# Performance work log

Hardware: AMD Instinct MI355X
Metric: run time of the kernel (lower is better)

## Reference

```python
import jax, jax.numpy as jnp
import numpy as np

N_NODES = 50000
N_EDGES = 800000
IN_DIM = 128
HIDDEN = 128
NUM_CLASSES = 2
NUM_GRAPHS = 512


def _linear_params(key, fan_in, fan_out):
    # torch nn.Linear default init: U(-1/sqrt(fan_in), 1/sqrt(fan_in))
    k1, k2 = jax.random.split(key)
    bound = 1.0 / np.sqrt(fan_in)
    W = jax.random.uniform(k1, (fan_in, fan_out), jnp.float32, -bound, bound)
    b = jax.random.uniform(k2, (fan_out,), jnp.float32, -bound, bound)
    return W, b


def setup_inputs() -> dict:
    key = jax.random.key(0)
    ks = jax.random.split(key, 8)
    x = jax.random.normal(ks[0], (N_NODES, IN_DIM), jnp.float32)
    edge_index = jax.random.randint(ks[1], (2, N_EDGES), 0, N_NODES, jnp.int64)
    batch = jnp.sort(jax.random.randint(ks[2], (N_NODES,), 0, NUM_GRAPHS, jnp.int64))
    W1a, b1a = _linear_params(ks[3], IN_DIM, HIDDEN)
    W1b, b1b = _linear_params(ks[4], HIDDEN, HIDDEN)
    W2a, b2a = _linear_params(ks[5], HIDDEN, HIDDEN)
    W2b, b2b = _linear_params(ks[6], HIDDEN, HIDDEN)
    Wfc, bfc = _linear_params(ks[7], HIDDEN, NUM_CLASSES)
    return {"x": x, "edge_index": edge_index, "batch": batch,
            "W1a": W1a, "b1a": b1a, "W1b": W1b, "b1b": b1b,
            "W2a": W2a, "b2a": b2a, "W2b": W2b, "b2b": b2b,
            "Wfc": Wfc, "bfc": bfc}


def _gin_layer(x, src, dst, Wa, ba, Wb, bb):
    # GINConv (eps=0): h_i = MLP(x_i + sum_{j->i} x_j)
    agg = jax.ops.segment_sum(x[src], dst, num_segments=N_NODES)
    h = x + agg
    h = jax.nn.relu(h @ Wa + ba)
    h = h @ Wb + bb
    return jax.nn.relu(h)  # outer F.relu in forward; dropout is identity (eval)


def reference(x, edge_index, batch, W1a, b1a, W1b, b1b, W2a, b2a, W2b, b2b, Wfc, bfc):
    src, dst = edge_index[0], edge_index[1]
    h = _gin_layer(x, src, dst, W1a, b1a, W1b, b1b)
    h = _gin_layer(h, src, dst, W2a, b2a, W2b, b2b)
    # global mean pool per graph
    sums = jax.ops.segment_sum(h, batch, num_segments=NUM_GRAPHS)
    counts = jax.ops.segment_sum(jnp.ones((N_NODES,), h.dtype), batch, num_segments=NUM_GRAPHS)
    g_emb = sums / jnp.maximum(counts, 1.0)[:, None]
    return g_emb @ Wfc + bfc  # [NUM_GRAPHS, NUM_CLASSES]
```

## Files before the change

kernel.cpp:

```cpp
#include <hip/hip_runtime.h>

typedef unsigned short ushort_t;
typedef unsigned int uint_t;

typedef __bf16 bf16x8 __attribute__((ext_vector_type(8)));
typedef float f32x4 __attribute__((ext_vector_type(4)));

#define N_NODES 50000
#define N_EDGES 800000
#define DIM 128
#define NUM_GRAPHS 512
#define LDA 136

#define ELL_CAP 64

#define EDGE_GROUPS 8
#define EDGE_BUCKET ((N_NODES + EDGE_GROUPS - 1) / EDGE_GROUPS)
#define EDGE_CHUNK 2048
#define EDGE_CHUNKS ((N_EDGES + EDGE_CHUNK - 1) / EDGE_CHUNK)
#define EDGE_BLOCKS (EDGE_CHUNKS * EDGE_GROUPS)

#define PREP_X_BLOCKS 6250
#define PREP_W_BLOCKS 256
#define PREP_B_BLOCKS 196
#define PREP_TOTAL (EDGE_BLOCKS + PREP_X_BLOCKS + PREP_W_BLOCKS + PREP_B_BLOCKS + 1)

__device__ __forceinline__ float bf2f(ushort_t u) {
    return __uint_as_float(((uint_t)u) << 16);
}
__device__ __forceinline__ ushort_t f2bf(float f) {
    uint_t u = __float_as_uint(f);
    u = (u + 0x7FFF + ((u >> 16) & 1)) >> 16;
    return (ushort_t)u;
}
__device__ __forceinline__ bf16x8 as_bf16x8(uint4 v) {
    return __builtin_bit_cast(bf16x8, v);
}

__global__ void zero_detect_kernel(int* cnt, float* gsum, const void* xraw,
                                   const void* eiraw, int* flags) {
    int i = blockIdx.x * 256 + threadIdx.x;
    if (i < N_NODES) cnt[i] = 0;
    if (i < NUM_GRAPHS * DIM) gsum[i] = 0.f;
    if (i == 0) {
        const ushort_t* u = (const ushort_t*)xraw;
        int extreme = 0;
        for (int k = 0; k < 128; ++k) {
            int e = (u[k] >> 7) & 0xFF;
            if (e >= 0xC0) extreme++;
        }
        flags[0] = (extreme > 8) ? 1 : 0;
        const int* p = (const int*)eiraw;
        int nonzero = 0;
        for (int k = 1; k < 64; k += 2) nonzero += (p[k] != 0);
        flags[1] = (nonzero == 0) ? 1 : 0;
    }
}

__global__ __launch_bounds__(256) void prep_all_kernel(
    const void* xraw, const void* braw, const void* eiraw,
    const void* W0, const void* W1, const void* W2, const void* W3,
    const void* pb1a, const void* pb1b, const void* pb2a, const void* pb2b,
    const void* pWfc, const void* pbfc, const int* __restrict__ flags,
    ushort_t* __restrict__ xout, ushort_t* __restrict__ wpout,
    int* __restrict__ batch32, float* __restrict__ params,
    int* __restrict__ cnt, int* __restrict__ ell) {
    int b = blockIdx.x;
    int tid = threadIdx.x;
    if (b < EDGE_BLOCKS) {
        int group = b & (EDGE_GROUPS - 1);
        int chunk = b >> 3;
        int lo = group * EDGE_BUCKET;
        int hi = lo + EDGE_BUCKET;
        const int* p = (const int*)eiraw;
        int i64 = flags[1];
#pragma unroll
        for (int i = 0; i < EDGE_CHUNK; i += 256) {
            int e = chunk * EDGE_CHUNK + i + tid;
            if (e < N_EDGES) {
                int d = i64 ? p[2 * (N_EDGES + e)] : p[N_EDGES + e];
                if (d >= lo && d < hi) {
                    int s = i64 ? p[2 * e] : p[e];
                    int slot = atomicAdd(&cnt[d], 1);
                    if (slot < ELL_CAP) ell[d * ELL_CAP + slot] = s;
                }
            }
        }
    } else if (b < EDGE_BLOCKS + PREP_X_BLOCKS) {
        if (flags[0]) {
            int i = (b - EDGE_BLOCKS) * 256 + tid;
            if (i < N_NODES * DIM / 4) {
                float4 v = ((const float4*)xraw)[i];
                ushort4 o;
                o.x = f2bf(v.x); o.y = f2bf(v.y); o.z = f2bf(v.z); o.w = f2bf(v.w);
                ((ushort4*)xout)[i] = o;
            }
        }
    } else if (b < EDGE_BLOCKS + PREP_X_BLOCKS + PREP_W_BLOCKS) {
        int gidx = (b - EDGE_BLOCKS - PREP_X_BLOCKS) * 256 + tid;
        int which = gidx >> 14;
        const void* W = (which == 0) ? W0 : (which == 1) ? W1 : (which == 2) ? W2 : W3;
        int idx = gidx & 16383;
        int j = idx & 7;
        int L = (idx >> 3) & 63;
        int t = (idx >> 9) & 7;
        int s = idx >> 12;
        int k = s * 32 + (L >> 4) * 8 + j;
        int n = t * 16 + (L & 15);
        int off = k * DIM + n;
        wpout[gidx] = flags[0] ? f2bf(((const float*)W)[off]) : ((const ushort_t*)W)[off];
    } else if (b < EDGE_BLOCKS + PREP_X_BLOCKS + PREP_W_BLOCKS + PREP_B_BLOCKS) {
        int i = (b - EDGE_BLOCKS - PREP_X_BLOCKS - PREP_W_BLOCKS) * 256 + tid;
        if (i < N_NODES) {
            const int* p = (const int*)braw;
            batch32[i] = flags[1] ? p[2 * i] : p[i];
        }
    } else {
        for (int i = tid; i < 770; i += 256) {
            const void* srcp;
            int j;
            if (i < 128)      { srcp = pb1a; j = i; }
            else if (i < 256) { srcp = pb1b; j = i - 128; }
            else if (i < 384) { srcp = pb2a; j = i - 256; }
            else if (i < 512) { srcp = pb2b; j = i - 384; }
            else if (i < 768) { srcp = pWfc; j = i - 512; }
            else              { srcp = pbfc; j = i - 768; }
            params[i] = flags[0] ? ((const float*)srcp)[j] : bf2f(((const ushort_t*)srcp)[j]);
        }
    }
}

__global__ __launch_bounds__(256) void agg_kernel(const ushort_t* __restrict__ featA,
                                                  const void* __restrict__ featB,
                                                  const int* __restrict__ flags,
                                                  const int* __restrict__ deg,
                                                  const int* __restrict__ ell,
                                                  ushort_t* __restrict__ hout) {
    int n = blockIdx.x * 16 + (threadIdx.x >> 4);
    int lane = threadIdx.x & 15;
    if (n >= N_NODES) return;
    const ushort_t* feat = featA;
    if (flags && !flags[0]) feat = (const ushort_t*)featB;
    const uint4* fp = reinterpret_cast<const uint4*>(feat);
    uint4 v = fp[(size_t)n * 16 + lane];
    float a0 = bf2f((ushort_t)(v.x & 0xffff));
    float a1 = bf2f((ushort_t)(v.x >> 16));
    float a2 = bf2f((ushort_t)(v.y & 0xffff));
    float a3 = bf2f((ushort_t)(v.y >> 16));
    float a4 = bf2f((ushort_t)(v.z & 0xffff));
    float a5 = bf2f((ushort_t)(v.z >> 16));
    float a6 = bf2f((ushort_t)(v.w & 0xffff));
    float a7 = bf2f((ushort_t)(v.w >> 16));
    int e1 = deg[n];
    if (e1 > ELL_CAP) e1 = ELL_CAP;
    const int* __restrict__ row = ell + (size_t)n * ELL_CAP;
    int j = 0;
#define ACC8(V) \
    a0 += bf2f((ushort_t)((V).x & 0xffff)); a1 += bf2f((ushort_t)((V).x >> 16)); \
    a2 += bf2f((ushort_t)((V).y & 0xffff)); a3 += bf2f((ushort_t)((V).y >> 16)); \
    a4 += bf2f((ushort_t)((V).z & 0xffff)); a5 += bf2f((ushort_t)((V).z >> 16)); \
    a6 += bf2f((ushort_t)((V).w & 0xffff)); a7 += bf2f((ushort_t)((V).w >> 16));
    for (; j + 8 <= e1; j += 8) {
        int s0 = row[j],     s1 = row[j + 1], s2 = row[j + 2], s3 = row[j + 3];
        int s4 = row[j + 4], s5 = row[j + 5], s6 = row[j + 6], s7 = row[j + 7];
        uint4 g0 = fp[(size_t)s0 * 16 + lane];
        uint4 g1 = fp[(size_t)s1 * 16 + lane];
        uint4 g2 = fp[(size_t)s2 * 16 + lane];
        uint4 g3 = fp[(size_t)s3 * 16 + lane];
        uint4 g4 = fp[(size_t)s4 * 16 + lane];
        uint4 g5 = fp[(size_t)s5 * 16 + lane];
        uint4 g6 = fp[(size_t)s6 * 16 + lane];
        uint4 g7 = fp[(size_t)s7 * 16 + lane];
        ACC8(g0) ACC8(g1) ACC8(g2) ACC8(g3)
        ACC8(g4) ACC8(g5) ACC8(g6) ACC8(g7)
    }
    for (; j + 4 <= e1; j += 4) {
        int s0 = row[j], s1 = row[j + 1], s2 = row[j + 2], s3 = row[j + 3];
        uint4 g0 = fp[(size_t)s0 * 16 + lane];
        uint4 g1 = fp[(size_t)s1 * 16 + lane];
        uint4 g2 = fp[(size_t)s2 * 16 + lane];
        uint4 g3 = fp[(size_t)s3 * 16 + lane];
        ACC8(g0) ACC8(g1) ACC8(g2) ACC8(g3)
    }
    for (; j < e1; ++j) {
        int s = row[j];
        uint4 g0 = fp[(size_t)s * 16 + lane];
        ACC8(g0)
    }
#undef ACC8
    uint4 o;
    o.x = (uint_t)f2bf(a0) | ((uint_t)f2bf(a1) << 16);
    o.y = (uint_t)f2bf(a2) | ((uint_t)f2bf(a3) << 16);
    o.z = (uint_t)f2bf(a4) | ((uint_t)f2bf(a5) << 16);
    o.w = (uint_t)f2bf(a6) | ((uint_t)f2bf(a7) << 16);
    reinterpret_cast<uint4*>(hout)[(size_t)n * 16 + lane] = o;
}

__global__ __launch_bounds__(256) void mlp_kernel(const ushort_t* __restrict__ hin,
                                                  const ushort_t* __restrict__ wpA,
                                                  const float* __restrict__ ba,
                                                  const ushort_t* __restrict__ wpB,
                                                  const float* __restrict__ bb,
                                                  ushort_t* __restrict__ hout) {
    __shared__ ushort_t As[64 * LDA];
    int tid = threadIdx.x;
    int wave = tid >> 6;
    int lane = tid & 63;
    int quad = lane >> 4;
    int cl = lane & 15;
    int row0 = blockIdx.x * 64;

    bf16x8 B1[2][4], B2[2][4];
#pragma unroll
    for (int ti = 0; ti < 2; ++ti) {
        int t = 2 * wave + ti;
#pragma unroll
        for (int s = 0; s < 4; ++s) {
            B1[ti][s] = as_bf16x8(reinterpret_cast<const uint4*>(wpA)[(s * 8 + t) * 64 + lane]);
            B2[ti][s] = as_bf16x8(reinterpret_cast<const uint4*>(wpB)[(s * 8 + t) * 64 + lane]);
        }
    }

    for (int i = tid; i < 64 * 16; i += 256) {
        int r = i >> 4, c8 = i & 15;
        uint4 v = make_uint4(0u, 0u, 0u, 0u);
        int gr = row0 + r;
        if (gr < N_NODES)
            v = reinterpret_cast<const uint4*>(hin + (size_t)gr * DIM)[c8];
        *reinterpret_cast<uint4*>(&As[r * LDA + c8 * 8]) = v;
    }
    __syncthreads();

    f32x4 acc[4][2];
#pragma unroll
    for (int m = 0; m < 4; ++m)
#pragma unroll
        for (int ti = 0; ti < 2; ++ti)
#pragma unroll
            for (int r = 0; r < 4; ++r) acc[m][ti][r] = 0.f;

#pragma unroll
    for (int s = 0; s < 4; ++s) {
#pragma unroll
        for (int m = 0; m < 4; ++m) {
            bf16x8 a = *reinterpret_cast<const bf16x8*>(&As[(m * 16 + cl) * LDA + s * 32 + quad * 8]);
#pragma unroll
            for (int ti = 0; ti < 2; ++ti)
                acc[m][ti] = __builtin_amdgcn_mfma_f32_16x16x32_bf16(a, B1[ti][s], acc[m][ti], 0, 0, 0);
        }
    }
    __syncthreads();

#pragma unroll
    for (int ti = 0; ti < 2; ++ti) {
        int col = 32 * wave + ti * 16 + cl;
        float bv = ba[col];
#pragma unroll
        for (int m = 0; m < 4; ++m)
#pragma unroll
            for (int r = 0; r < 4; ++r) {
                float v = acc[m][ti][r] + bv;
                As[(m * 16 + quad * 4 + r) * LDA + col] = f2bf(fmaxf(v, 0.f));
            }
    }
    __syncthreads();

#pragma unroll
    for (int m = 0; m < 4; ++m)
#pragma unroll
        for (int ti = 0; ti < 2; ++ti)
#pragma unroll
            for (int r = 0; r < 4; ++r) acc[m][ti][r] = 0.f;

#pragma unroll
    for (int s = 0; s < 4; ++s) {
#pragma unroll
        for (int m = 0; m < 4; ++m) {
            bf16x8 a = *reinterpret_cast<const bf16x8*>(&As[(m * 16 + cl) * LDA + s * 32 + quad * 8]);
#pragma unroll
            for (int ti = 0; ti < 2; ++ti)
                acc[m][ti] = __builtin_amdgcn_mfma_f32_16x16x32_bf16(a, B2[ti][s], acc[m][ti], 0, 0, 0);
        }
    }

#pragma unroll
    for (int ti = 0; ti < 2; ++ti) {
        int col = 32 * wave + ti * 16 + cl;
        float bv = bb[col];
#pragma unroll
        for (int m = 0; m < 4; ++m)
#pragma unroll
            for (int r = 0; r < 4; ++r) {
                int gr = row0 + m * 16 + quad * 4 + r;
                if (gr < N_NODES) {
                    float v = acc[m][ti][r] + bv;
                    hout[(size_t)gr * DIM + col] = f2bf(fmaxf(v, 0.f));
                }
            }
    }
}

__global__ __launch_bounds__(256) void mlp_pool_kernel(const ushort_t* __restrict__ hin,
                                                       const ushort_t* __restrict__ wpA,
                                                       const float* __restrict__ ba,
                                                       const ushort_t* __restrict__ wpB,
                                                       const float* __restrict__ bb,
                                                       const int* __restrict__ batch32,
                                                       float* __restrict__ gsum) {
    __shared__ ushort_t As[64 * LDA];
    int tid = threadIdx.x;
    int wave = tid >> 6;
    int lane = tid & 63;
    int quad = lane >> 4;
    int cl = lane & 15;
    int row0 = blockIdx.x * 64;

    bf16x8 B1[2][4], B2[2][4];
#pragma unroll
    for (int ti = 0; ti < 2; ++ti) {
        int t = 2 * wave + ti;
#pragma unroll
        for (int s = 0; s < 4; ++s) {
            B1[ti][s] = as_bf16x8(reinterpret_cast<const uint4*>(wpA)[(s * 8 + t) * 64 + lane]);
            B2[ti][s] = as_bf16x8(reinterpret_cast<const uint4*>(wpB)[(s * 8 + t) * 64 + lane]);
        }
    }

    for (int i = tid; i < 64 * 16; i += 256) {
        int r = i >> 4, c8 = i & 15;
        uint4 v = make_uint4(0u, 0u, 0u, 0u);
        int gr = row0 + r;
        if (gr < N_NODES)
            v = reinterpret_cast<const uint4*>(hin + (size_t)gr * DIM)[c8];
        *reinterpret_cast<uint4*>(&As[r * LDA + c8 * 8]) = v;
    }
    __syncthreads();

    f32x4 acc[4][2];
#pragma unroll
    for (int m = 0; m < 4; ++m)
#pragma unroll
        for (int ti = 0; ti < 2; ++ti)
#pragma unroll
            for (int r = 0; r < 4; ++r) acc[m][ti][r] = 0.f;

#pragma unroll
    for (int s = 0; s < 4; ++s) {
#pragma unroll
        for (int m = 0; m < 4; ++m) {
            bf16x8 a = *reinterpret_cast<const bf16x8*>(&As[(m * 16 + cl) * LDA + s * 32 + quad * 8]);
#pragma unroll
            for (int ti = 0; ti < 2; ++ti)
                acc[m][ti] = __builtin_amdgcn_mfma_f32_16x16x32_bf16(a, B1[ti][s], acc[m][ti], 0, 0, 0);
        }
    }
    __syncthreads();

#pragma unroll
    for (int ti = 0; ti < 2; ++ti) {
        int col = 32 * wave + ti * 16 + cl;
        float bv = ba[col];
#pragma unroll
        for (int m = 0; m < 4; ++m)
#pragma unroll
            for (int r = 0; r < 4; ++r) {
                float v = acc[m][ti][r] + bv;
                As[(m * 16 + quad * 4 + r) * LDA + col] = f2bf(fmaxf(v, 0.f));
            }
    }
    __syncthreads();

#pragma unroll
    for (int m = 0; m < 4; ++m)
#pragma unroll
        for (int ti = 0; ti < 2; ++ti)
#pragma unroll
            for (int r = 0; r < 4; ++r) acc[m][ti][r] = 0.f;

#pragma unroll
    for (int s = 0; s < 4; ++s) {
#pragma unroll
        for (int m = 0; m < 4; ++m) {
            bf16x8 a = *reinterpret_cast<const bf16x8*>(&As[(m * 16 + cl) * LDA + s * 32 + quad * 8]);
#pragma unroll
            for (int ti = 0; ti < 2; ++ti)
                acc[m][ti] = __builtin_amdgcn_mfma_f32_16x16x32_bf16(a, B2[ti][s], acc[m][ti], 0, 0, 0);
        }
    }
    __syncthreads();

#pragma unroll
    for (int ti = 0; ti < 2; ++ti) {
        int col = 32 * wave + ti * 16 + cl;
        float bv = bb[col];
#pragma unroll
        for (int m = 0; m < 4; ++m)
#pragma unroll
            for (int r = 0; r < 4; ++r) {
                float v = acc[m][ti][r] + bv;
                As[(m * 16 + quad * 4 + r) * LDA + col] = f2bf(fmaxf(v, 0.f));
            }
    }
    __syncthreads();

    int c = tid & 127;
    int rbase = (tid >> 7) * 32;
    float accp = 0.f;
    int curg = -1;
    for (int r = rbase; r < rbase + 32; ++r) {
        int gr = row0 + r;
        if (gr >= N_NODES) break;
        int g = batch32[gr];
        if (g != curg) {
            if (curg >= 0) atomicAdd(&gsum[curg * DIM + c], accp);
            curg = g;
            accp = 0.f;
        }
        accp += bf2f(As[r * LDA + c]);
    }
    if (curg >= 0) atomicAdd(&gsum[curg * DIM + c], accp);
}

__global__ __launch_bounds__(64) void fc_kernel(const float* __restrict__ gsum,
                                                const int* __restrict__ batch,
                                                const float* __restrict__ params,
                                                const int* __restrict__ flags,
                                                void* __restrict__ out) {
    int g = blockIdx.x;
    int l = threadIdx.x;
    int lo = 0, hi = N_NODES;
    while (lo < hi) { int mid = (lo + hi) >> 1; if (batch[mid] < g) lo = mid + 1; else hi = mid; }
    int start = lo;
    hi = N_NODES;
    while (lo < hi) { int mid = (lo + hi) >> 1; if (batch[mid] < g + 1) lo = mid + 1; else hi = mid; }
    int cnt = lo - start;
    float inv = 1.0f / (float)(cnt > 0 ? cnt : 1);
    float m0 = gsum[g * DIM + l] * inv;
    float m1 = gsum[g * DIM + 64 + l] * inv;
    float p0 = m0 * params[512 + l * 2 + 0] + m1 * params[512 + (64 + l) * 2 + 0];
    float p1 = m0 * params[512 + l * 2 + 1] + m1 * params[512 + (64 + l) * 2 + 1];
#pragma unroll
    for (int off = 32; off > 0; off >>= 1) {
        p0 += __shfl_down(p0, off, 64);
        p1 += __shfl_down(p1, off, 64);
    }
    if (l == 0) {
        float o0 = p0 + params[768];
        float o1 = p1 + params[769];
        if (flags[0]) {
            ((float*)out)[g * 2 + 0] = o0;
            ((float*)out)[g * 2 + 1] = o1;
        } else {
            ((ushort_t*)out)[g * 2 + 0] = f2bf(o0);
            ((ushort_t*)out)[g * 2 + 1] = f2bf(o1);
        }
    }
}

extern "C" void kernel_launch(void* const* d_in, const int* in_sizes, int n_in,
                              void* d_out, int out_size, void* d_ws, size_t ws_size,
                              hipStream_t stream) {
    const void* x = d_in[0];
    const void* ei = d_in[1];
    const void* batch = d_in[2];
    const void* W1a = d_in[3];
    const void* b1a = d_in[4];
    const void* W1b = d_in[5];
    const void* b1b = d_in[6];
    const void* W2a = d_in[7];
    const void* b2a = d_in[8];
    const void* W2b = d_in[9];
    const void* b2b = d_in[10];
    const void* Wfc = d_in[11];
    const void* bfc = d_in[12];

    char* base = (char*)d_ws;
    ushort_t* hX = (ushort_t*)base;   base += (size_t)N_NODES * DIM * 2;
    ushort_t* hA = (ushort_t*)base;   base += (size_t)N_NODES * DIM * 2;
    int* ell = (int*)base;            base += (size_t)N_NODES * ELL_CAP * 4;
    int* cnt = (int*)base;            base += (size_t)N_NODES * 4;
    int* batch32 = (int*)base;        base += (size_t)N_NODES * 4;
    ushort_t* wp = (ushort_t*)base;   base += 4 * 16384 * 2;
    float* params = (float*)base;     base += 772 * 4;
    float* gsum = (float*)base;       base += (size_t)NUM_GRAPHS * DIM * 4;
    int* flags = (int*)base;          base += 16;

    ushort_t* wpA1 = wp;
    ushort_t* wpB1 = wp + 16384;
    ushort_t* wpA2 = wp + 2 * 16384;
    ushort_t* wpB2 = wp + 3 * 16384;

    zero_detect_kernel<<<256, 256, 0, stream>>>(cnt, gsum, x, ei, flags);
    prep_all_kernel<<<PREP_TOTAL, 256, 0, stream>>>(x, batch, ei, W1a, W1b, W2a, W2b,
                                                    b1a, b1b, b2a, b2b, Wfc, bfc, flags,
                                                    hX, wp, batch32, params, cnt, ell);

    agg_kernel<<<(N_NODES + 15) / 16, 256, 0, stream>>>(hX, x, flags, cnt, ell, hA);
    mlp_kernel<<<(N_NODES + 63) / 64, 256, 0, stream>>>(hA, wpA1, params + 0, wpB1, params + 128, hA);
    agg_kernel<<<(N_NODES + 15) / 16, 256, 0, stream>>>(hA, hA, nullptr, cnt, ell, hX);
    mlp_pool_kernel<<<(N_NODES + 63) / 64, 256, 0, stream>>>(hX, wpA2, params + 256, wpB2, params + 384,
                                                             batch32, gsum);
    fc_kernel<<<NUM_GRAPHS, 64, 0, stream>>>(gsum, batch32, params, flags, d_out);
}
```

Measured before the change: 240.7 us.

## Two-pass bucketed ELL build via per-group FIFOs and separate scatter kernel

Edge adjacency construction is split into two passes. The first pass reads each edge once, bins it by destination group with shared-memory counters, and appends (src,dst) pairs to per-group FIFOs. A new scatter kernel then fills the ELL rows from each group's FIFO with better locality. This replaces the old scheme where every chunk was read eight times, once per group. The aggregation kernel also loads neighbor indices as int4 vectors. The cost is an extra kernel launch, an extra round trip of edge pairs through memory, and a FIFO capacity that silently drops edges if a group overflows.

```diff
diff --git a/kernel.cpp b/kernel.cpp
--- a/kernel.cpp
+++ b/kernel.cpp
@@ -16,14 +16,16 @@
 
 #define EDGE_GROUPS 8
 #define EDGE_BUCKET ((N_NODES + EDGE_GROUPS - 1) / EDGE_GROUPS)
-#define EDGE_CHUNK 2048
-#define EDGE_CHUNKS ((N_EDGES + EDGE_CHUNK - 1) / EDGE_CHUNK)
-#define EDGE_BLOCKS (EDGE_CHUNKS * EDGE_GROUPS)
+#define A_CHUNK 2048
+#define A_BLOCKS ((N_EDGES + A_CHUNK - 1) / A_CHUNK)
+#define FIFO_CAP 110592
 
 #define PREP_X_BLOCKS 6250
 #define PREP_W_BLOCKS 256
 #define PREP_B_BLOCKS 196
-#define PREP_TOTAL (EDGE_BLOCKS + PREP_X_BLOCKS + PREP_W_BLOCKS + PREP_B_BLOCKS + 1)
+#define PREP_TOTAL (A_BLOCKS + PREP_X_BLOCKS + PREP_W_BLOCKS + PREP_B_BLOCKS + 1)
+
+#define SCATTER_BLOCKS 512
 
 __device__ __forceinline__ float bf2f(ushort_t u) {
     return __uint_as_float(((uint_t)u) << 16);
@@ -37,11 +39,12 @@
     return __builtin_bit_cast(bf16x8, v);
 }
 
-__global__ void zero_detect_kernel(int* cnt, float* gsum, const void* xraw,
+__global__ void zero_detect_kernel(int* cnt, float* gsum, int* gcnt, const void* xraw,
                                    const void* eiraw, int* flags) {
     int i = blockIdx.x * 256 + threadIdx.x;
     if (i < N_NODES) cnt[i] = 0;
     if (i < NUM_GRAPHS * DIM) gsum[i] = 0.f;
+    if (i < EDGE_GROUPS) gcnt[i] = 0;
     if (i == 0) {
         const ushort_t* u = (const ushort_t*)xraw;
         int extreme = 0;
@@ -64,31 +67,46 @@
     const void* pWfc, const void* pbfc, const int* __restrict__ flags,
     ushort_t* __restrict__ xout, ushort_t* __restrict__ wpout,
     int* __restrict__ batch32, float* __restrict__ params,
-    int* __restrict__ cnt, int* __restrict__ ell) {
+    int* __restrict__ gcnt, int2* __restrict__ fifo) {
+    __shared__ int lcnt[EDGE_GROUPS];
+    __shared__ int lbase[EDGE_GROUPS];
     int b = blockIdx.x;
     int tid = threadIdx.x;
-    if (b < EDGE_BLOCKS) {
-        int group = b & (EDGE_GROUPS - 1);
-        int chunk = b >> 3;
-        int lo = group * EDGE_BUCKET;
-        int hi = lo + EDGE_BUCKET;
+    if (b < A_BLOCKS) {
+        if (tid < EDGE_GROUPS) lcnt[tid] = 0;
+        __syncthreads();
         const int* p = (const int*)eiraw;
         int i64 = flags[1];
-#pragma unroll
-        for (int i = 0; i < EDGE_CHUNK; i += 256) {
-            int e = chunk * EDGE_CHUNK + i + tid;
-            if (e < N_EDGES) {
-                int d = i64 ? p[2 * (N_EDGES + e)] : p[N_EDGES + e];
-                if (d >= lo && d < hi) {
-                    int s = i64 ? p[2 * e] : p[e];
-                    int slot = atomicAdd(&cnt[d], 1);
-                    if (slot < ELL_CAP) ell[d * ELL_CAP + slot] = s;
-                }
-            }
-        }
-    } else if (b < EDGE_BLOCKS + PREP_X_BLOCKS) {
+        int base_e = b * A_CHUNK;
+        int g[8], r[8], sv[8], dv[8];
+#pragma unroll
+        for (int k = 0; k < 8; ++k) {
+            int e = base_e + k * 256 + tid;
+            int valid = e < N_EDGES;
+            int s = 0, d = 0;
+            if (valid) {
+                if (i64) { s = p[2 * e]; d = p[2 * (N_EDGES + e)]; }
+                else     { s = p[e];     d = p[N_EDGES + e]; }
+            }
+            sv[k] = s; dv[k] = d;
+            g[k] = valid ? (d / EDGE_BUCKET) : -1;
+            r[k] = 0;
+            if (valid) r[k] = atomicAdd(&lcnt[g[k]], 1);
+        }
+        __syncthreads();
+        if (tid < EDGE_GROUPS) lbase[tid] = atomicAdd(&gcnt[tid], lcnt[tid]);
+        __syncthreads();
+#pragma unroll
+        for (int k = 0; k < 8; ++k) {
+            if (g[k] >= 0) {
+                int pos = lbase[g[k]] + r[k];
+                if (pos < FIFO_CAP)
+                    fifo[(size_t)g[k] * FIFO_CAP + pos] = make_int2(sv[k], dv[k]);
+            }
+        }
+    } else if (b < A_BLOCKS + PREP_X_BLOCKS) {
         if (flags[0]) {
-            int i = (b - EDGE_BLOCKS) * 256 + tid;
+            int i = (b - A_BLOCKS) * 256 + tid;
             if (i < N_NODES * DIM / 4) {
                 float4 v = ((const float4*)xraw)[i];
                 ushort4 o;
@@ -96,8 +114,8 @@
                 ((ushort4*)xout)[i] = o;
             }
         }
-    } else if (b < EDGE_BLOCKS + PREP_X_BLOCKS + PREP_W_BLOCKS) {
-        int gidx = (b - EDGE_BLOCKS - PREP_X_BLOCKS) * 256 + tid;
+    } else if (b < A_BLOCKS + PREP_X_BLOCKS + PREP_W_BLOCKS) {
+        int gidx = (b - A_BLOCKS - PREP_X_BLOCKS) * 256 + tid;
         int which = gidx >> 14;
         const void* W = (which == 0) ? W0 : (which == 1) ? W1 : (which == 2) ? W2 : W3;
         int idx = gidx & 16383;
@@ -109,8 +127,8 @@
         int n = t * 16 + (L & 15);
         int off = k * DIM + n;
         wpout[gidx] = flags[0] ? f2bf(((const float*)W)[off]) : ((const ushort_t*)W)[off];
-    } else if (b < EDGE_BLOCKS + PREP_X_BLOCKS + PREP_W_BLOCKS + PREP_B_BLOCKS) {
-        int i = (b - EDGE_BLOCKS - PREP_X_BLOCKS - PREP_W_BLOCKS) * 256 + tid;
+    } else if (b < A_BLOCKS + PREP_X_BLOCKS + PREP_W_BLOCKS + PREP_B_BLOCKS) {
+        int i = (b - A_BLOCKS - PREP_X_BLOCKS - PREP_W_BLOCKS) * 256 + tid;
         if (i < N_NODES) {
             const int* p = (const int*)braw;
             batch32[i] = flags[1] ? p[2 * i] : p[i];
@@ -127,6 +145,22 @@
             else              { srcp = pbfc; j = i - 768; }
             params[i] = flags[0] ? ((const float*)srcp)[j] : bf2f(((const ushort_t*)srcp)[j]);
         }
+    }
+}
+
+__global__ __launch_bounds__(256) void scatter_kernel(const int2* __restrict__ fifo,
+                                                      const int* __restrict__ gcnt,
+                                                      int* __restrict__ cnt,
+                                                      int* __restrict__ ell) {
+    int g = blockIdx.x & (EDGE_GROUPS - 1);
+    int sub = blockIdx.x >> 3;
+    int n = gcnt[g];
+    if (n > FIFO_CAP) n = FIFO_CAP;
+    const int2* f = fifo + (size_t)g * FIFO_CAP;
+    for (int i = sub * 256 + threadIdx.x; i < n; i += (SCATTER_BLOCKS / EDGE_GROUPS) * 256) {
+        int2 sd = f[i];
+        int slot = atomicAdd(&cnt[sd.y], 1);
+        if (slot < ELL_CAP) ell[sd.y * ELL_CAP + slot] = sd.x;
     }
 }
 
@@ -153,6 +187,7 @@
     float a7 = bf2f((ushort_t)(v.w >> 16));
     int e1 = deg[n];
     if (e1 > ELL_CAP) e1 = ELL_CAP;
+    const int4* __restrict__ rp4 = reinterpret_cast<const int4*>(ell + (size_t)n * ELL_CAP);
     const int* __restrict__ row = ell + (size_t)n * ELL_CAP;
     int j = 0;
 #define ACC8(V) \
@@ -161,25 +196,25 @@
     a4 += bf2f((ushort_t)((V).z & 0xffff)); a5 += bf2f((ushort_t)((V).z >> 16)); \
     a6 += bf2f((ushort_t)((V).w & 0xffff)); a7 += bf2f((ushort_t)((V).w >> 16));
     for (; j + 8 <= e1; j += 8) {
-        int s0 = row[j],     s1 = row[j + 1], s2 = row[j + 2], s3 = row[j + 3];
-        int s4 = row[j + 4], s5 = row[j + 5], s6 = row[j + 6], s7 = row[j + 7];
-        uint4 g0 = fp[(size_t)s0 * 16 + lane];
-        uint4 g1 = fp[(size_t)s1 * 16 + lane];
-        uint4 g2 = fp[(size_t)s2 * 16 + lane];
-        uint4 g3 = fp[(size_t)s3 * 16 + lane];
-        uint4 g4 = fp[(size_t)s4 * 16 + lane];
-        uint4 g5 = fp[(size_t)s5 * 16 + lane];
-        uint4 g6 = fp[(size_t)s6 * 16 + lane];
-        uint4 g7 = fp[(size_t)s7 * 16 + lane];
+        int4 ra = rp4[j >> 2];
+        int4 rb = rp4[(j >> 2) + 1];
+        uint4 g0 = fp[(size_t)ra.x * 16 + lane];
+        uint4 g1 = fp[(size_t)ra.y * 16 + lane];
+        uint4 g2 = fp[(size_t)ra.z * 16 + lane];
+        uint4 g3 = fp[(size_t)ra.w * 16 + lane];
+        uint4 g4 = fp[(size_t)rb.x * 16 + lane];
+        uint4 g5 = fp[(size_t)rb.y * 16 + lane];
+        uint4 g6 = fp[(size_t)rb.z * 16 + lane];
+        uint4 g7 = fp[(size_t)rb.w * 16 + lane];
         ACC8(g0) ACC8(g1) ACC8(g2) ACC8(g3)
         ACC8(g4) ACC8(g5) ACC8(g6) ACC8(g7)
     }
     for (; j + 4 <= e1; j += 4) {
-        int s0 = row[j], s1 = row[j + 1], s2 = row[j + 2], s3 = row[j + 3];
-        uint4 g0 = fp[(size_t)s0 * 16 + lane];
-        uint4 g1 = fp[(size_t)s1 * 16 + lane];
-        uint4 g2 = fp[(size_t)s2 * 16 + lane];
-        uint4 g3 = fp[(size_t)s3 * 16 + lane];
+        int4 ra = rp4[j >> 2];
+        uint4 g0 = fp[(size_t)ra.x * 16 + lane];
+        uint4 g1 = fp[(size_t)ra.y * 16 + lane];
+        uint4 g2 = fp[(size_t)ra.z * 16 + lane];
+        uint4 g3 = fp[(size_t)ra.w * 16 + lane];
         ACC8(g0) ACC8(g1) ACC8(g2) ACC8(g3)
     }
     for (; j < e1; ++j) {
@@ -478,8 +513,10 @@
     ushort_t* hX = (ushort_t*)base;   base += (size_t)N_NODES * DIM * 2;
     ushort_t* hA = (ushort_t*)base;   base += (size_t)N_NODES * DIM * 2;
     int* ell = (int*)base;            base += (size_t)N_NODES * ELL_CAP * 4;
+    int2* fifo = (int2*)base;         base += (size_t)EDGE_GROUPS * FIFO_CAP * 8;
     int* cnt = (int*)base;            base += (size_t)N_NODES * 4;
     int* batch32 = (int*)base;        base += (size_t)N_NODES * 4;
+    int* gcnt = (int*)base;           base += 64;
     ushort_t* wp = (ushort_t*)base;   base += 4 * 16384 * 2;
     float* params = (float*)base;     base += 772 * 4;
     float* gsum = (float*)base;       base += (size_t)NUM_GRAPHS * DIM * 4;
@@ -490,10 +527,11 @@
     ushort_t* wpA2 = wp + 2 * 16384;
     ushort_t* wpB2 = wp + 3 * 16384;
 
-    zero_detect_kernel<<<256, 256, 0, stream>>>(cnt, gsum, x, ei, flags);
+    zero_detect_kernel<<<256, 256, 0, stream>>>(cnt, gsum, gcnt, x, ei, flags);
     prep_all_kernel<<<PREP_TOTAL, 256, 0, stream>>>(x, batch, ei, W1a, W1b, W2a, W2b,
                                                     b1a, b1b, b2a, b2b, Wfc, bfc, flags,
-                                                    hX, wp, batch32, params, cnt, ell);
+                                                    hX, wp, batch32, params, gcnt, fifo);
+    scatter_kernel<<<SCATTER_BLOCKS, 256, 0, stream>>>(fifo, gcnt, cnt, ell);
 
     agg_kernel<<<(N_NODES + 15) / 16, 256, 0, stream>>>(hX, x, flags, cnt, ell, hA);
     mlp_kernel<<<(N_NODES + 63) / 64, 256, 0, stream>>>(hA, wpA1, params + 0, wpB1, params + 128, hA);
```

After: 247.5 us. +2.8%, slower.
